# Kernel tuning notes

Measured on AMD Instinct MI355X. Metric: run time of the kernel, lower is better.

Reference implementation:

```python
import jax, jax.numpy as jnp
import numpy as np

N_LIG, N_TGT, E = 100000, 20000, 250000
LIG_IN, TGT_IN, H = 4, 1280, 128


def setup_inputs() -> dict:
    key = jax.random.key(0)
    ks = jax.random.split(key, 12)
    def lin_w(k, fan_in, fan_out):
        # kaiming-uniform-ish init, stored as [in, out] for x @ W
        bound = 1.0 / np.sqrt(fan_in)
        return jax.random.uniform(k, (fan_in, fan_out), jnp.float32, -bound, bound)
    return {
        "x_ligand": jax.random.normal(ks[0], (N_LIG, LIG_IN), jnp.float32),
        "x_target": jax.random.normal(ks[1], (N_TGT, TGT_IN), jnp.float32),
        "edge_src": jax.random.randint(ks[2], (E,), 0, N_LIG, jnp.int32),
        "edge_dst": jax.random.randint(ks[3], (E,), 0, N_TGT, jnp.int32),
        # SAGEConv (ligand -> target): lin_l on aggregated ligand msgs, lin_r on target self
        "W_lt_l": lin_w(ks[4], LIG_IN, H),
        "b_lt_l": jnp.zeros((H,), jnp.float32),
        "W_lt_r": lin_w(ks[5], TGT_IN, H),
        # SAGEConv (target -> ligand): lin_l on aggregated target msgs, lin_r on ligand self
        "W_tl_l": lin_w(ks[6], TGT_IN, H),
        "b_tl_l": jnp.zeros((H,), jnp.float32),
        "W_tl_r": lin_w(ks[7], LIG_IN, H),
        # edge predictor: Linear(2H -> 1)
        "W_ep": lin_w(ks[8], 2 * H, 1),
        "b_ep": jnp.zeros((1,), jnp.float32),
    }


def _mean_agg(x_src, src_idx, dst_idx, num_dst):
    # gather per-edge source features, scatter-mean onto destination nodes
    msg = x_src[src_idx]                                             # [E, F]
    s = jax.ops.segment_sum(msg, dst_idx, num_segments=num_dst)      # [N_dst, F]
    cnt = jax.ops.segment_sum(jnp.ones((src_idx.shape[0], 1), x_src.dtype),
                              dst_idx, num_segments=num_dst)         # [N_dst, 1]
    return s / jnp.maximum(cnt, 1.0)


def reference(x_ligand, x_target, edge_src, edge_dst,
              W_lt_l, b_lt_l, W_lt_r, W_tl_l, b_tl_l, W_tl_r, W_ep, b_ep):
    # SAGEConv (ligand, binds_to, target): aggregate ligand msgs into targets
    agg_t = _mean_agg(x_ligand, edge_src, edge_dst, N_TGT)           # [N_TGT, LIG_IN]
    t_out = agg_t @ W_lt_l + b_lt_l + x_target @ W_lt_r              # [N_TGT, H]
    # SAGEConv (target, binds_to, ligand): reversed edges (flip(0))
    agg_l = _mean_agg(x_target, edge_dst, edge_src, N_LIG)           # [N_LIG, TGT_IN]
    l_out = agg_l @ W_tl_l + b_tl_l + x_ligand @ W_tl_r              # [N_LIG, H]
    l_out = jax.nn.relu(l_out)
    t_out = jax.nn.relu(t_out)
    # edge predictor: gather endpoints, concat, linear, squeeze
    edge_feats = jnp.concatenate([l_out[edge_src], t_out[edge_dst]], axis=-1)  # [E, 2H]
    out = (edge_feats @ W_ep + b_ep).squeeze(-1)                     # [E]
    return out
```

## Files before the change

### kernel.cpp

```cpp
#include <hip/hip_runtime.h>
#include <hip/hip_bf16.h>


#define H 128
#define K_DIM 1280
#define LIG_IN 4
#define CAP_L 24
#define CAP_T 48

typedef __attribute__((ext_vector_type(8))) short bf16x8;
typedef __attribute__((ext_vector_type(4))) float f32x4;

#define AS1(p) ((const __attribute__((address_space(1))) void*)(p))
#define AS3(p) ((__attribute__((address_space(3))) void*)(p))

__global__ void fill_both(const int* __restrict__ src, const int* __restrict__ dst,
                          int* __restrict__ cur_l, int* __restrict__ cur_t,
                          int* __restrict__ adjd, int* __restrict__ adjs, int E)
{
    int e = blockIdx.x * blockDim.x + threadIdx.x;
    if (e >= E) return;
    int s = src[e], d = dst[e];
    int p = atomicAdd(&cur_l[s], 1);
    adjd[s * CAP_L + p] = d;
    int q = atomicAdd(&cur_t[d], 1);
    adjs[d * CAP_T + q] = s;
}

__global__ void cast_wt(const float* __restrict__ Wl, const float* __restrict__ Wr,
                        __hip_bfloat16* __restrict__ Wt, int n)
{
    int idx = blockIdx.x * blockDim.x + threadIdx.x;
    if (idx >= n) return;
    int nr = idx / K_DIM, k = idx - nr * K_DIM;
    float v = (nr < H) ? Wl[k * H + nr] : Wr[k * H + (nr - H)];
    Wt[idx] = __float2bfloat16(v);
}

__global__ __launch_bounds__(256)
void gemm_fused(const float* __restrict__ Xf,
                const unsigned short* __restrict__ Wt,
                float* __restrict__ y_tl, float* __restrict__ t_lin, int M)
{
    __shared__ short As[2][32 * 32];
    __shared__ short Bs[2][256 * 32];

    const int bm = blockIdx.x * 32;
    const int t = threadIdx.x;
    const int w = t >> 6, lane = t & 63;
    const int mrow = lane & 15, quad = lane >> 4;

    const int a_row = t >> 3, a_seg = t & 7;
    const float* gA = Xf + (size_t)(bm + a_row) * K_DIM + a_seg * 4;
    const int lA_off = a_row * 64 + a_seg * 8;

    const unsigned short* gB[4];
    int lB_off[4];
#pragma unroll
    for (int r = 0; r < 4; ++r) {
        int row = w * 64 + r * 16 + (lane >> 2);
        int seg = lane & 3;
        gB[r] = Wt + (size_t)row * K_DIM + seg * 8;
        lB_off[r] = w * 4096 + r * 1024 + lane * 16;
    }

    f32x4 acc[2][4];
#pragma unroll
    for (int i = 0; i < 2; ++i)
#pragma unroll
        for (int j = 0; j < 4; ++j)
            acc[i][j] = (f32x4){0.f, 0.f, 0.f, 0.f};

#pragma unroll
    for (int r = 0; r < 4; ++r)
        __builtin_amdgcn_global_load_lds(AS1(gB[r]), AS3((char*)Bs[0] + lB_off[r]), 16, 0, 0);
    {
        float4 v = *(const float4*)gA;
        union { __hip_bfloat16 h[4]; uint2 u; } c;
        c.h[0] = __float2bfloat16(v.x); c.h[1] = __float2bfloat16(v.y);
        c.h[2] = __float2bfloat16(v.z); c.h[3] = __float2bfloat16(v.w);
        *(uint2*)((char*)As[0] + lA_off) = c.u;
    }
    __syncthreads();

    const int NK = K_DIM / 32;
    for (int k = 0; k < NK; ++k) {
        const int cur = k & 1, nxt = cur ^ 1;
        float4 vn;
        if (k + 1 < NK) {
#pragma unroll
            for (int r = 0; r < 4; ++r)
                __builtin_amdgcn_global_load_lds(AS1(gB[r] + (k + 1) * 32),
                                                 AS3((char*)Bs[nxt] + lB_off[r]), 16, 0, 0);
            vn = *(const float4*)(gA + (k + 1) * 32);
        }

        bf16x8 aF[2], bF[4];
#pragma unroll
        for (int i = 0; i < 2; ++i)
            aF[i] = *(const bf16x8*)((const char*)As[cur] + (i * 16 + mrow) * 64 + quad * 16);
#pragma unroll
        for (int j = 0; j < 4; ++j)
            bF[j] = *(const bf16x8*)((const char*)Bs[cur] + (w * 64 + j * 16 + mrow) * 64 + quad * 16);
#pragma unroll
        for (int i = 0; i < 2; ++i)
#pragma unroll
            for (int j = 0; j < 4; ++j)
                acc[i][j] = __builtin_amdgcn_mfma_f32_16x16x32_bf16(aF[i], bF[j], acc[i][j], 0, 0, 0);

        if (k + 1 < NK) {
            union { __hip_bfloat16 h[4]; uint2 u; } c;
            c.h[0] = __float2bfloat16(vn.x); c.h[1] = __float2bfloat16(vn.y);
            c.h[2] = __float2bfloat16(vn.z); c.h[3] = __float2bfloat16(vn.w);
            *(uint2*)((char*)As[nxt] + lA_off) = c.u;
        }
        __syncthreads();
    }

    float* __restrict__ Y = (w < 2) ? y_tl : t_lin;
    const int cbase = (w & 1) * 64;
#pragma unroll
    for (int i = 0; i < 2; ++i) {
#pragma unroll
        for (int r = 0; r < 4; ++r) {
            int row = bm + i * 16 + quad * 4 + r;
#pragma unroll
            for (int j = 0; j < 4; ++j) {
                int col = cbase + j * 16 + mrow;
                Y[(size_t)row * H + col] = acc[i][j][r];
            }
        }
    }
}

__global__ void target_post(const int* __restrict__ cur_t, const int* __restrict__ adjs,
                            const float* __restrict__ xl, const float* __restrict__ t_lin,
                            const float* __restrict__ W_lt_l, const float* __restrict__ b_lt_l,
                            const float* __restrict__ W_ep,
                            float* __restrict__ st, int NT)
{
    int wid = (blockIdx.x * blockDim.x + threadIdx.x) >> 6;
    int lane = threadIdx.x & 63;
    if (wid >= NT) return;
    int cnt = cur_t[wid];
    float a0 = 0.f, a1 = 0.f, a2 = 0.f, a3 = 0.f;
    for (int j = lane; j < cnt; j += 64) {
        int s = adjs[wid * CAP_T + j];
        float4 v = *(const float4*)(xl + (size_t)s * LIG_IN);
        a0 += v.x; a1 += v.y; a2 += v.z; a3 += v.w;
    }
#pragma unroll
    for (int off = 32; off > 0; off >>= 1) {
        a0 += __shfl_xor(a0, off);
        a1 += __shfl_xor(a1, off);
        a2 += __shfl_xor(a2, off);
        a3 += __shfl_xor(a3, off);
    }
    float inv = 1.0f / fmaxf((float)cnt, 1.0f);
    a0 *= inv; a1 *= inv; a2 *= inv; a3 *= inv;
    float acc = 0.f;
#pragma unroll
    for (int p = 0; p < 2; ++p) {
        int h = lane + p * 64;
        float v = a0 * W_lt_l[h] + a1 * W_lt_l[H + h] + a2 * W_lt_l[2 * H + h] +
                  a3 * W_lt_l[3 * H + h] + b_lt_l[h] + t_lin[(size_t)wid * H + h];
        v = fmaxf(v, 0.f);
        acc += v * W_ep[H + h];
    }
#pragma unroll
    for (int off = 32; off > 0; off >>= 1) acc += __shfl_down(acc, off);
    if (lane == 0) st[wid] = acc;
}

__global__ void ligand_gather_post(const int* __restrict__ cur_l, const int* __restrict__ adjd,
                                   const float* __restrict__ y_tl,
                                   const float* __restrict__ xl,
                                   const float* __restrict__ W_tl_r, const float* __restrict__ b_tl_l,
                                   const float* __restrict__ W_ep,
                                   float* __restrict__ sl, int NL)
{
    int wid = (blockIdx.x * blockDim.x + threadIdx.x) >> 6;
    int lane = threadIdx.x & 63;
    if (wid >= NL) return;
    int cnt = cur_l[wid];
    float a0 = 0.f, a1 = 0.f;
    for (int j = 0; j < cnt; ++j) {
        int d = adjd[wid * CAP_L + j];
        float2 f = ((const float2*)(y_tl + (size_t)d * H))[lane];
        a0 += f.x;
        a1 += f.y;
    }
    float inv = 1.0f / fmaxf((float)cnt, 1.0f);
    float4 x = *(const float4*)(xl + (size_t)wid * LIG_IN);
    float acc = 0.f;
    {
        int h = 2 * lane;
        float v = a0 * inv + b_tl_l[h] +
                  x.x * W_tl_r[h] + x.y * W_tl_r[H + h] +
                  x.z * W_tl_r[2 * H + h] + x.w * W_tl_r[3 * H + h];
        v = fmaxf(v, 0.f);
        acc += v * W_ep[h];
    }
    {
        int h = 2 * lane + 1;
        float v = a1 * inv + b_tl_l[h] +
                  x.x * W_tl_r[h] + x.y * W_tl_r[H + h] +
                  x.z * W_tl_r[2 * H + h] + x.w * W_tl_r[3 * H + h];
        v = fmaxf(v, 0.f);
        acc += v * W_ep[h];
    }
#pragma unroll
    for (int off = 32; off > 0; off >>= 1) acc += __shfl_down(acc, off);
    if (lane == 0) sl[wid] = acc;
}

__global__ void edge_out(const int* __restrict__ src, const int* __restrict__ dst,
                         const float* __restrict__ sl, const float* __restrict__ st,
                         const float* __restrict__ b_ep, float* __restrict__ out, int E)
{
    int e = blockIdx.x * blockDim.x + threadIdx.x;
    if (e >= E) return;
    out[e] = sl[src[e]] + st[dst[e]] + b_ep[0];
}

extern "C" void kernel_launch(void* const* d_in, const int* in_sizes, int n_in,
                              void* d_out, int out_size, void* d_ws, size_t ws_size,
                              hipStream_t stream) {
    const float* x_ligand = (const float*)d_in[0];
    const float* x_target = (const float*)d_in[1];
    const int*   edge_src = (const int*)d_in[2];
    const int*   edge_dst = (const int*)d_in[3];
    const float* W_lt_l   = (const float*)d_in[4];
    const float* b_lt_l   = (const float*)d_in[5];
    const float* W_lt_r   = (const float*)d_in[6];
    const float* W_tl_l   = (const float*)d_in[7];
    const float* b_tl_l   = (const float*)d_in[8];
    const float* W_tl_r   = (const float*)d_in[9];
    const float* W_ep     = (const float*)d_in[10];
    const float* b_ep     = (const float*)d_in[11];
    float* out = (float*)d_out;

    const int NL = in_sizes[0] / LIG_IN;
    const int NT = in_sizes[1] / K_DIM;
    const int E  = in_sizes[2];

    char* ws = (char*)d_ws;
    size_t off = 0;
    auto take = [&](size_t bytes) { size_t o = off; off += (bytes + 15) & ~(size_t)15; return o; };
    size_t off_Wt     = take((size_t)2 * H * K_DIM * 2);
    size_t off_y_tl   = take((size_t)NT * H * 4);
    size_t off_t_lin  = take((size_t)NT * H * 4);
    size_t off_adjd   = take((size_t)NL * CAP_L * 4);
    size_t off_adjs   = take((size_t)NT * CAP_T * 4);
    size_t off_cur_l  = take((size_t)NL * 4);
    size_t off_cur_t  = take((size_t)NT * 4);
    size_t off_sl     = take((size_t)NL * 4);
    size_t off_st     = take((size_t)NT * 4);
    if (off > ws_size) {
        hipMemsetAsync(d_out, 0, (size_t)out_size * 4, stream);
        return;
    }

    __hip_bfloat16* Wt = (__hip_bfloat16*)(ws + off_Wt);
    float* y_tl  = (float*)(ws + off_y_tl);
    float* t_lin = (float*)(ws + off_t_lin);
    int*   adjd  = (int*)(ws + off_adjd);
    int*   adjs  = (int*)(ws + off_adjs);
    int*   cur_l = (int*)(ws + off_cur_l);
    int*   cur_t = (int*)(ws + off_cur_t);
    float* sl    = (float*)(ws + off_sl);
    float* st    = (float*)(ws + off_st);

    hipMemsetAsync(cur_l, 0, off_sl - off_cur_l, stream);

    int nw = 2 * H * K_DIM;
    cast_wt<<<(nw + 255) / 256, 256, 0, stream>>>(W_tl_l, W_lt_r, Wt, nw);

    gemm_fused<<<NT / 32, 256, 0, stream>>>(x_target, (const unsigned short*)Wt, y_tl, t_lin, NT);

    fill_both<<<(E + 255) / 256, 256, 0, stream>>>(edge_src, edge_dst,
                                                   cur_l, cur_t, adjd, adjs, E);

    target_post<<<(NT * 64 + 255) / 256, 256, 0, stream>>>(cur_t, adjs, x_ligand, t_lin,
                                                           W_lt_l, b_lt_l, W_ep, st, NT);
    ligand_gather_post<<<(NL * 64 + 255) / 256, 256, 0, stream>>>(cur_l, adjd, y_tl, x_ligand,
                                                                  W_tl_r, b_tl_l, W_ep, sl, NL);
    edge_out<<<(E + 255) / 256, 256, 0, stream>>>(edge_src, edge_dst, sl, st, b_ep, out, E);
}
```

Before: 319.6 us.

## Restructure fused GEMM with 64-row tiles, register A, and swizzled 128-K LDS chunks

The dense x_target GEMM now uses 64-row blocks in which each wave owns 16 rows and all 256 output columns. A is read straight from global into registers, double-buffered, and converted to bf16 in registers, so the LDS staging for A is gone. B is staged in 128-wide K chunks with an XOR swizzle to avoid LDS bank conflicts, which cuts the number of barriers from 40 to about 20. This raises per-block B reuse and accumulator register pressure (16 f32x4 per lane). B loads are no longer overlapped with compute, since each chunk is fetched after a barrier.

```diff
diff --git a/kernel.cpp b/kernel.cpp
--- a/kernel.cpp
+++ b/kernel.cpp
@@ -37,98 +37,95 @@
     Wt[idx] = __float2bfloat16(v);
 }
 
-__global__ __launch_bounds__(256)
+__device__ inline bf16x8 cvt8(float4 u, float4 v)
+{
+    union { __hip_bfloat16 h[8]; bf16x8 f; } r;
+    r.h[0] = __float2bfloat16(u.x); r.h[1] = __float2bfloat16(u.y);
+    r.h[2] = __float2bfloat16(u.z); r.h[3] = __float2bfloat16(u.w);
+    r.h[4] = __float2bfloat16(v.x); r.h[5] = __float2bfloat16(v.y);
+    r.h[6] = __float2bfloat16(v.z); r.h[7] = __float2bfloat16(v.w);
+    return r.f;
+}
+
+#define NCHUNK 10
+__global__ __launch_bounds__(256, 2)
 void gemm_fused(const float* __restrict__ Xf,
                 const unsigned short* __restrict__ Wt,
                 float* __restrict__ y_tl, float* __restrict__ t_lin, int M)
 {
-    __shared__ short As[2][32 * 32];
-    __shared__ short Bs[2][256 * 32];
-
-    const int bm = blockIdx.x * 32;
+    __shared__ short Bs[256 * 128];
+
     const int t = threadIdx.x;
     const int w = t >> 6, lane = t & 63;
-    const int mrow = lane & 15, quad = lane >> 4;
-
-    const int a_row = t >> 3, a_seg = t & 7;
-    const float* gA = Xf + (size_t)(bm + a_row) * K_DIM + a_seg * 4;
-    const int lA_off = a_row * 64 + a_seg * 8;
-
-    const unsigned short* gB[4];
-    int lB_off[4];
-#pragma unroll
-    for (int r = 0; r < 4; ++r) {
-        int row = w * 64 + r * 16 + (lane >> 2);
-        int seg = lane & 3;
-        gB[r] = Wt + (size_t)row * K_DIM + seg * 8;
-        lB_off[r] = w * 4096 + r * 1024 + lane * 16;
-    }
-
-    f32x4 acc[2][4];
-#pragma unroll
-    for (int i = 0; i < 2; ++i)
-#pragma unroll
-        for (int j = 0; j < 4; ++j)
-            acc[i][j] = (f32x4){0.f, 0.f, 0.f, 0.f};
-
-#pragma unroll
-    for (int r = 0; r < 4; ++r)
-        __builtin_amdgcn_global_load_lds(AS1(gB[r]), AS3((char*)Bs[0] + lB_off[r]), 16, 0, 0);
-    {
-        float4 v = *(const float4*)gA;
-        union { __hip_bfloat16 h[4]; uint2 u; } c;
-        c.h[0] = __float2bfloat16(v.x); c.h[1] = __float2bfloat16(v.y);
-        c.h[2] = __float2bfloat16(v.z); c.h[3] = __float2bfloat16(v.w);
-        *(uint2*)((char*)As[0] + lA_off) = c.u;
+    const int m = lane & 15, q = lane >> 4;
+    const int bm = blockIdx.x * 64;
+
+    const int rowc = min(bm + w * 16 + m, M - 1);
+    const float* gA = Xf + (size_t)rowc * K_DIM + q * 8;
+
+    f32x4 acc[16];
+#pragma unroll
+    for (int j = 0; j < 16; ++j) acc[j] = (f32x4){0.f, 0.f, 0.f, 0.f};
+
+    float4 a4[2][8];
+
+#pragma unroll
+    for (int s = 0; s < 4; ++s) {
+        a4[0][2 * s]     = *(const float4*)(gA + s * 32);
+        a4[0][2 * s + 1] = *(const float4*)(gA + s * 32 + 4);
+    }
+#pragma unroll
+    for (int i = 0; i < 16; ++i) {
+        int L = i * 256 + t;
+        int n = L >> 4, cp = L & 15;
+        int cc = cp ^ (n & 15);
+        __builtin_amdgcn_global_load_lds(AS1(Wt + (size_t)n * K_DIM + cc * 8),
+                                         AS3((char*)Bs + (i * 256 + w * 64) * 16), 16, 0, 0);
     }
     __syncthreads();
 
-    const int NK = K_DIM / 32;
-    for (int k = 0; k < NK; ++k) {
-        const int cur = k & 1, nxt = cur ^ 1;
-        float4 vn;
-        if (k + 1 < NK) {
-#pragma unroll
-            for (int r = 0; r < 4; ++r)
-                __builtin_amdgcn_global_load_lds(AS1(gB[r] + (k + 1) * 32),
-                                                 AS3((char*)Bs[nxt] + lB_off[r]), 16, 0, 0);
-            vn = *(const float4*)(gA + (k + 1) * 32);
-        }
-
-        bf16x8 aF[2], bF[4];
-#pragma unroll
-        for (int i = 0; i < 2; ++i)
-            aF[i] = *(const bf16x8*)((const char*)As[cur] + (i * 16 + mrow) * 64 + quad * 16);
-#pragma unroll
-        for (int j = 0; j < 4; ++j)
-            bF[j] = *(const bf16x8*)((const char*)Bs[cur] + (w * 64 + j * 16 + mrow) * 64 + quad * 16);
-#pragma unroll
-        for (int i = 0; i < 2; ++i)
-#pragma unroll
-            for (int j = 0; j < 4; ++j)
-                acc[i][j] = __builtin_amdgcn_mfma_f32_16x16x32_bf16(aF[i], bF[j], acc[i][j], 0, 0, 0);
-
-        if (k + 1 < NK) {
-            union { __hip_bfloat16 h[4]; uint2 u; } c;
-            c.h[0] = __float2bfloat16(vn.x); c.h[1] = __float2bfloat16(vn.y);
-            c.h[2] = __float2bfloat16(vn.z); c.h[3] = __float2bfloat16(vn.w);
-            *(uint2*)((char*)As[nxt] + lA_off) = c.u;
+    for (int c = 0; c < NCHUNK; ++c) {
+        const int cur = c & 1;
+        if (c + 1 < NCHUNK) {
+#pragma unroll
+            for (int s = 0; s < 4; ++s) {
+                a4[cur ^ 1][2 * s]     = *(const float4*)(gA + (c + 1) * 128 + s * 32);
+                a4[cur ^ 1][2 * s + 1] = *(const float4*)(gA + (c + 1) * 128 + s * 32 + 4);
+            }
+        }
+#pragma unroll
+        for (int s = 0; s < 4; ++s) {
+            bf16x8 aF = cvt8(a4[cur][2 * s], a4[cur][2 * s + 1]);
+#pragma unroll
+            for (int j = 0; j < 16; ++j) {
+                bf16x8 bF = *(const bf16x8*)((const char*)Bs +
+                              (j * 16 + m) * 256 + (((s * 4 + q) ^ m) * 16));
+                acc[j] = __builtin_amdgcn_mfma_f32_16x16x32_bf16(aF, bF, acc[j], 0, 0, 0);
+            }
         }
         __syncthreads();
-    }
-
-    float* __restrict__ Y = (w < 2) ? y_tl : t_lin;
-    const int cbase = (w & 1) * 64;
-#pragma unroll
-    for (int i = 0; i < 2; ++i) {
+        if (c + 1 < NCHUNK) {
+            const int kc = (c + 1) * 128;
+#pragma unroll
+            for (int i = 0; i < 16; ++i) {
+                int L = i * 256 + t;
+                int n = L >> 4, cp = L & 15;
+                int cc = cp ^ (n & 15);
+                __builtin_amdgcn_global_load_lds(AS1(Wt + (size_t)n * K_DIM + kc + cc * 8),
+                                                 AS3((char*)Bs + (i * 256 + w * 64) * 16), 16, 0, 0);
+            }
+            __syncthreads();
+        }
+    }
+
+#pragma unroll
+    for (int j = 0; j < 16; ++j) {
+        float* __restrict__ Y = (j < 8) ? y_tl : t_lin;
+        int col = (j & 7) * 16 + m;
 #pragma unroll
         for (int r = 0; r < 4; ++r) {
-            int row = bm + i * 16 + quad * 4 + r;
-#pragma unroll
-            for (int j = 0; j < 4; ++j) {
-                int col = cbase + j * 16 + mrow;
-                Y[(size_t)row * H + col] = acc[i][j][r];
-            }
+            int row = bm + w * 16 + q * 4 + r;
+            if (row < M) Y[(size_t)row * H + col] = acc[j][r];
         }
     }
 }
@@ -276,7 +273,8 @@
     int nw = 2 * H * K_DIM;
     cast_wt<<<(nw + 255) / 256, 256, 0, stream>>>(W_tl_l, W_lt_r, Wt, nw);
 
-    gemm_fused<<<NT / 32, 256, 0, stream>>>(x_target, (const unsigned short*)Wt, y_tl, t_lin, NT);
+    gemm_fused<<<(NT + 63) / 64, 256, 0, stream>>>(x_target, (const unsigned short*)Wt,
+                                                   y_tl, t_lin, NT);
 
     fill_both<<<(E + 255) / 256, 256, 0, stream>>>(edge_src, edge_dst,
                                                    cur_l, cur_t, adjd, adjs, E);
```

After: 358.3 us. 1.12x slower.
